# Kernel optimization log

Hardware: AMD Instinct MI355X
Metric: run time of the kernel (lower is better)

Reference implementation:

```python
import jax, jax.numpy as jnp
import numpy as np

N_NODES = 100000
N_EDGES = 1600000
IN_C = 64
HID = 64


def _glorot(key, shape):
    fan_in, fan_out = shape[1], shape[0]
    lim = (6.0 / (fan_in + fan_out)) ** 0.5
    return jax.random.uniform(key, shape, jnp.float32, -lim, lim)


def setup_inputs() -> dict:
    key = jax.random.key(0)
    ks = jax.random.split(key, 8)
    x = jax.random.normal(ks[0], (N_NODES, IN_C), jnp.float32)
    edge_index = jax.random.randint(ks[1], (2, N_EDGES), 0, N_NODES, jnp.int32)
    return {
        "x": x,
        "edge_index": edge_index,
        # conv1 (SAGEConv in->hid): lin_l (bias), lin_r (no bias)
        "W1l": _glorot(ks[2], (HID, IN_C)),
        "b1l": jnp.zeros((HID,), jnp.float32),
        "W1r": _glorot(ks[3], (HID, IN_C)),
        # conv2 (SAGEConv hid->hid)
        "W2l": _glorot(ks[4], (HID, HID)),
        "b2l": jnp.zeros((HID,), jnp.float32),
        "W2r": _glorot(ks[5], (HID, HID)),
        # edge scorer: Linear(2*hid, 1)
        "Wlin": _glorot(ks[6], (1, 2 * HID)),
        "blin": jnp.zeros((1,), jnp.float32),
    }


def _sage_conv(x, src, dst, Wl, bl, Wr, n_nodes):
    # mean aggregation of source features onto destination nodes
    agg = jax.ops.segment_sum(x[src], dst, num_segments=n_nodes)  # [N, F]
    cnt = jax.ops.segment_sum(jnp.ones((src.shape[0],), x.dtype), dst,
                              num_segments=n_nodes)  # [N]
    mean = agg / jnp.maximum(cnt, 1.0)[:, None]  # isolated nodes -> 0
    return mean @ Wl.T + bl + x @ Wr.T


def reference(x, edge_index, W1l, b1l, W1r, W2l, b2l, W2r, Wlin, blin):
    src, dst = edge_index[0], edge_index[1]
    n = x.shape[0]
    h = jax.nn.relu(_sage_conv(x, src, dst, W1l, b1l, W1r, n))
    h = jax.nn.relu(_sage_conv(h, src, dst, W2l, b2l, W2r, n))
    he = jnp.concatenate([h[src], h[dst]], axis=1)  # [E, 2*HID]
    return (he @ Wlin.T + blin).squeeze(-1)  # [E]
```

## Files before the change

kernel.cpp:

```cpp
#include <hip/hip_runtime.h>
#include <hip/hip_bf16.h>

#define N_NODES 100000
#define N_EDGES 1600000
#define NBUCK 196
#define BCAP 12288
#define CHUNK 4096
#define PART_BLOCKS 391
#define CONV_BLOCKS 6250
#define CAP32 32
#define QNODES 128
#define QCAP 3072
#define MSTRIDE 36


typedef __hip_bfloat16 bf16;
typedef short short8 __attribute__((ext_vector_type(8)));
typedef float f32x4 __attribute__((ext_vector_type(4)));
typedef unsigned int uint;

__device__ __forceinline__ short f2bs(float f) {
    bf16 h = __float2bfloat16(f);
    short s; __builtin_memcpy(&s, &h, 2); return s;
}
__device__ __forceinline__ float lo_bf(uint w) {
    uint v = w << 16; float f; __builtin_memcpy(&f, &v, 4); return f;
}
__device__ __forceinline__ float hi_bf(uint w) {
    uint v = w & 0xFFFF0000u; float f; __builtin_memcpy(&f, &v, 4); return f;
}
__device__ __forceinline__ uint pack2(float a, float b) {
    return (uint)(unsigned short)f2bs(a) | ((uint)(unsigned short)f2bs(b) << 16);
}
__device__ __forceinline__ short8 load8bf(const bf16* __restrict__ p, long idx) {
    return *(const short8*)((const short*)p + idx);
}

__global__ __launch_bounds__(256) void prep_kernel(
    const float* __restrict__ x, bf16* __restrict__ xb,
    const float* __restrict__ W1l, const float* __restrict__ W1r,
    const float* __restrict__ W2l, const float* __restrict__ W2r,
    bf16* __restrict__ wb,
    const int* __restrict__ src, const int* __restrict__ dst,
    int* __restrict__ gcur, int* __restrict__ pk)
{
    __shared__ int pl[256 * CAP32];
    __shared__ int cnt[256], gb[256];
    int t = threadIdx.x;

    if (blockIdx.x >= PART_BLOCKS) {
        int cb = blockIdx.x - PART_BLOCKS;
        int i = cb * 256 + t;
        float4 v = ((const float4*)x)[i];
        uint2 o;
        o.x = pack2(v.x, v.y);
        o.y = pack2(v.z, v.w);
        ((uint2*)xb)[i] = o;
        if (cb == 0) {
            for (int k = t; k < 16384; k += 256) {
                float vv;
                if (k < 4096)       vv = W1l[k];
                else if (k < 8192)  vv = W1r[k - 4096];
                else if (k < 12288) vv = W2l[k - 8192];
                else                vv = W2r[k - 12288];
                wb[k] = __float2bfloat16(vv);
            }
        }
        return;
    }

    cnt[t] = 0;
    __syncthreads();
    int e0 = blockIdx.x * CHUNK;
    for (int i = t; i < CHUNK; i += 256) {
        int e = e0 + i;
        if (e < N_EDGES) {
            int d = dst[e];
            int b = d >> 9;
            int payload = src[e] | ((d & 511) << 17);
            int p = atomicAdd(&cnt[b], 1);
            if (p < CAP32) {
                pl[b * CAP32 + p] = payload;
            } else {
                int g = atomicAdd(&gcur[b], 1);
                if (g < BCAP) pk[b * BCAP + g] = payload;
            }
        }
    }
    __syncthreads();
    {
        int c = cnt[t] < CAP32 ? cnt[t] : CAP32;
        gb[t] = c > 0 ? atomicAdd(&gcur[t], c) : 0;
        cnt[t] = c;
    }
    __syncthreads();
    for (int i = t; i < 256 * CAP32; i += 256) {
        int b = i >> 5;
        int pos = i & (CAP32 - 1);
        if (pos < cnt[b]) {
            int g = gb[b] + pos;
            if (g < BCAP) pk[b * BCAP + g] = pl[i];
        }
    }
}

__global__ __launch_bounds__(512) void csr_build(
    const int* __restrict__ gcur, const int* __restrict__ pk,
    int* __restrict__ csr, int2* __restrict__ node_range)
{
    __shared__ int deg[512], scn[512];
    __shared__ int cur[QNODES];
    __shared__ int csr_l[QCAP];
    int t = threadIdx.x;
    int b = blockIdx.x >> 2;
    int q = blockIdx.x & 3;
    int base = b * BCAP;
    int cnt = gcur[b];
    if (cnt > BCAP) cnt = BCAP;
    deg[t] = 0;
    __syncthreads();
    for (int i = t; i < cnt; i += 512)
        atomicAdd(&deg[pk[base + i] >> 17], 1);
    __syncthreads();
    if (t < 64) {
        int e[8], inc[8], s = 0;
#pragma unroll
        for (int k = 0; k < 8; k++) { e[k] = deg[t * 8 + k]; s += e[k]; inc[k] = s; }
        int run = s;
#pragma unroll
        for (int off = 1; off < 64; off <<= 1) {
            int u = __shfl_up(run, off);
            if (t >= off) run += u;
        }
        int excl = run - s;
#pragma unroll
        for (int k = 0; k < 8; k++) scn[t * 8 + k] = excl + inc[k];
    }
    __syncthreads();
    int hs = q * QNODES;
    int hend = hs + QNODES;
    int hs_excl = scn[hs] - deg[hs];
    int he_excl = (hend < 512) ? (scn[hend] - deg[hend]) : cnt;
    int qcnt = he_excl - hs_excl;
    int excl = scn[t] - deg[t];
    if (t >= hs && t < hend) {
        cur[t - hs] = excl - hs_excl;
        int n = (b << 9) + t;
        if (n < N_NODES) node_range[n] = make_int2(base + excl, base + excl + deg[t]);
    }
    __syncthreads();
    for (int i = t; i < cnt; i += 512) {
        int v = pk[base + i];
        int ld = v >> 17;
        if (ld >= hs && ld < hend) {
            int p = atomicAdd(&cur[ld - hs], 1);
            if (p < QCAP) csr_l[p] = v & 0x1FFFF;
        }
    }
    __syncthreads();
    for (int i = t; i < qcnt && i < QCAP; i += 512)
        csr[base + hs_excl + i] = csr_l[i];
}


__device__ __forceinline__ void gather_mean_lds(
    const bf16* __restrict__ feat, const int2* __restrict__ node_range,
    const int* __restrict__ csr, int nb0, uint* __restrict__ mean_l)
{
    int wave = threadIdx.x >> 6, lane = threadIdx.x & 63;
    int g = lane >> 3, ci = lane & 7;
    int nl = wave * 8 + g;
    int n = nb0 + nl;
    int2 rg = (n < N_NODES) ? node_range[n] : make_int2(0, 0);
    int beg = rg.x, end = rg.y;
    const uint* fw = (const uint*)feat;
    float a0 = 0.f, a1 = 0.f, a2 = 0.f, a3 = 0.f;
    float a4 = 0.f, a5 = 0.f, a6 = 0.f, a7 = 0.f;
    int i = beg;
    for (; i + 7 < end; i += 8) {
        int s0 = csr[i],     s1 = csr[i + 1], s2 = csr[i + 2], s3 = csr[i + 3];
        int s4 = csr[i + 4], s5 = csr[i + 5], s6 = csr[i + 6], s7 = csr[i + 7];
        uint4 w0 = *(const uint4*)(fw + (long)s0 * 32 + ci * 4);
        uint4 w1 = *(const uint4*)(fw + (long)s1 * 32 + ci * 4);
        uint4 w2 = *(const uint4*)(fw + (long)s2 * 32 + ci * 4);
        uint4 w3 = *(const uint4*)(fw + (long)s3 * 32 + ci * 4);
        uint4 w4 = *(const uint4*)(fw + (long)s4 * 32 + ci * 4);
        uint4 w5 = *(const uint4*)(fw + (long)s5 * 32 + ci * 4);
        uint4 w6 = *(const uint4*)(fw + (long)s6 * 32 + ci * 4);
        uint4 w7 = *(const uint4*)(fw + (long)s7 * 32 + ci * 4);
        a0 += lo_bf(w0.x) + lo_bf(w1.x) + lo_bf(w2.x) + lo_bf(w3.x)
            + lo_bf(w4.x) + lo_bf(w5.x) + lo_bf(w6.x) + lo_bf(w7.x);
        a1 += hi_bf(w0.x) + hi_bf(w1.x) + hi_bf(w2.x) + hi_bf(w3.x)
            + hi_bf(w4.x) + hi_bf(w5.x) + hi_bf(w6.x) + hi_bf(w7.x);
        a2 += lo_bf(w0.y) + lo_bf(w1.y) + lo_bf(w2.y) + lo_bf(w3.y)
            + lo_bf(w4.y) + lo_bf(w5.y) + lo_bf(w6.y) + lo_bf(w7.y);
        a3 += hi_bf(w0.y) + hi_bf(w1.y) + hi_bf(w2.y) + hi_bf(w3.y)
            + hi_bf(w4.y) + hi_bf(w5.y) + hi_bf(w6.y) + hi_bf(w7.y);
        a4 += lo_bf(w0.z) + lo_bf(w1.z) + lo_bf(w2.z) + lo_bf(w3.z)
            + lo_bf(w4.z) + lo_bf(w5.z) + lo_bf(w6.z) + lo_bf(w7.z);
        a5 += hi_bf(w0.z) + hi_bf(w1.z) + hi_bf(w2.z) + hi_bf(w3.z)
            + hi_bf(w4.z) + hi_bf(w5.z) + hi_bf(w6.z) + hi_bf(w7.z);
        a6 += lo_bf(w0.w) + lo_bf(w1.w) + lo_bf(w2.w) + lo_bf(w3.w)
            + lo_bf(w4.w) + lo_bf(w5.w) + lo_bf(w6.w) + lo_bf(w7.w);
        a7 += hi_bf(w0.w) + hi_bf(w1.w) + hi_bf(w2.w) + hi_bf(w3.w)
            + hi_bf(w4.w) + hi_bf(w5.w) + hi_bf(w6.w) + hi_bf(w7.w);
    }
    for (; i + 1 < end; i += 2) {
        int s0 = csr[i], s1 = csr[i + 1];
        uint4 w0 = *(const uint4*)(fw + (long)s0 * 32 + ci * 4);
        uint4 w1 = *(const uint4*)(fw + (long)s1 * 32 + ci * 4);
        a0 += lo_bf(w0.x) + lo_bf(w1.x); a1 += hi_bf(w0.x) + hi_bf(w1.x);
        a2 += lo_bf(w0.y) + lo_bf(w1.y); a3 += hi_bf(w0.y) + hi_bf(w1.y);
        a4 += lo_bf(w0.z) + lo_bf(w1.z); a5 += hi_bf(w0.z) + hi_bf(w1.z);
        a6 += lo_bf(w0.w) + lo_bf(w1.w); a7 += hi_bf(w0.w) + hi_bf(w1.w);
    }
    if (i < end) {
        int s = csr[i];
        uint4 w = *(const uint4*)(fw + (long)s * 32 + ci * 4);
        a0 += lo_bf(w.x); a1 += hi_bf(w.x);
        a2 += lo_bf(w.y); a3 += hi_bf(w.y);
        a4 += lo_bf(w.z); a5 += hi_bf(w.z);
        a6 += lo_bf(w.w); a7 += hi_bf(w.w);
    }
    int d = end - beg;
    float inv = d > 0 ? 1.0f / (float)d : 0.0f;
    uint4 qv;
    qv.x = pack2(a0 * inv, a1 * inv);
    qv.y = pack2(a2 * inv, a3 * inv);
    qv.z = pack2(a4 * inv, a5 * inv);
    qv.w = pack2(a6 * inv, a7 * inv);
    *(uint4*)(mean_l + nl * MSTRIDE + ci * 4) = qv;
}

__device__ __forceinline__ short8 load_bfrag(
    const bf16* __restrict__ wlb, int f, int c, int quad)
{
    if (c < 2) return load8bf(wlb, (long)f * 64 + c * 32 + quad * 8);
    return load8bf(wlb, 4096 + (long)f * 64 + (c - 2) * 32 + quad * 8);
}

__global__ __launch_bounds__(512) void layer1_fused(
    const bf16* __restrict__ xb, const int2* __restrict__ nrng,
    const int* __restrict__ csr, const bf16* __restrict__ wlb,
    const float* __restrict__ bl, bf16* __restrict__ h_out)
{
    __shared__ uint mean_l[64 * MSTRIDE];
    int nb0 = blockIdx.x * 64;
    gather_mean_lds(xb, nrng, csr, nb0, mean_l);
    __syncthreads();
    int tid = threadIdx.x;
    int wave = tid >> 6, lane = tid & 63;
    if (wave >= 4) return;
    int quad = lane >> 4, n16 = lane & 15;
    int nb = nb0 + wave * 16;
    int ln = wave * 16 + n16;

    int node_a = nb + n16;
    int na = node_a < N_NODES ? node_a : N_NODES - 1;
    short8 a[4];
#pragma unroll
    for (int c = 0; c < 2; c++)
        a[c] = *(const short8*)(mean_l + ln * MSTRIDE + c * 16 + quad * 4);
#pragma unroll
    for (int c = 0; c < 2; c++)
        a[2 + c] = load8bf(xb, (long)na * 64 + c * 32 + quad * 8);

#pragma unroll
    for (int t = 0; t < 4; t++) {
        int f = 16 * t + n16;
        f32x4 acc = {0.f, 0.f, 0.f, 0.f};
#pragma unroll
        for (int c = 0; c < 4; c++) {
            short8 b = load_bfrag(wlb, f, c, quad);
            acc = __builtin_amdgcn_mfma_f32_16x16x32_bf16(a[c], b, acc, 0, 0, 0);
        }
        float bias = bl[f];
#pragma unroll
        for (int r = 0; r < 4; r++) {
            int node = nb + quad * 4 + r;
            if (node < N_NODES)
                h_out[(long)node * 64 + f] = __float2bfloat16(fmaxf(acc[r] + bias, 0.0f));
        }
    }
}

__global__ __launch_bounds__(512) void layer2_fused(
    const bf16* __restrict__ h1, const int2* __restrict__ nrng,
    const int* __restrict__ csr, const bf16* __restrict__ wlb,
    const float* __restrict__ bl, const float* __restrict__ Wlin,
    float* __restrict__ s_src, float* __restrict__ s_dst)
{
    __shared__ uint mean_l[64 * MSTRIDE];
    int nb0 = blockIdx.x * 64;
    gather_mean_lds(h1, nrng, csr, nb0, mean_l);
    __syncthreads();
    int tid = threadIdx.x;
    int wave = tid >> 6, lane = tid & 63;
    if (wave >= 4) return;
    int quad = lane >> 4, n16 = lane & 15;
    int nb = nb0 + wave * 16;
    int ln = wave * 16 + n16;

    int node_a = nb + n16;
    int na = node_a < N_NODES ? node_a : N_NODES - 1;
    short8 a[4];
#pragma unroll
    for (int c = 0; c < 2; c++)
        a[c] = *(const short8*)(mean_l + ln * MSTRIDE + c * 16 + quad * 4);
#pragma unroll
    for (int c = 0; c < 2; c++)
        a[2 + c] = load8bf(h1, (long)na * 64 + c * 32 + quad * 8);

    float sa[4] = {0.f, 0.f, 0.f, 0.f};
    float sb[4] = {0.f, 0.f, 0.f, 0.f};
#pragma unroll
    for (int t = 0; t < 4; t++) {
        int f = 16 * t + n16;
        f32x4 acc = {0.f, 0.f, 0.f, 0.f};
#pragma unroll
        for (int c = 0; c < 4; c++) {
            short8 b = load_bfrag(wlb, f, c, quad);
            acc = __builtin_amdgcn_mfma_f32_16x16x32_bf16(a[c], b, acc, 0, 0, 0);
        }
        float bias = bl[f];
        float wa = Wlin[f];
        float wb = Wlin[64 + f];
#pragma unroll
        for (int r = 0; r < 4; r++) {
            float h = fmaxf(acc[r] + bias, 0.0f);
            sa[r] += h * wa;
            sb[r] += h * wb;
        }
    }
#pragma unroll
    for (int m = 1; m < 16; m <<= 1) {
#pragma unroll
        for (int r = 0; r < 4; r++) {
            sa[r] += __shfl_xor(sa[r], m);
            sb[r] += __shfl_xor(sb[r], m);
        }
    }
    if (n16 == 0) {
#pragma unroll
        for (int r = 0; r < 4; r++) {
            int node = nb + quad * 4 + r;
            if (node < N_NODES) { s_src[node] = sa[r]; s_dst[node] = sb[r]; }
        }
    }
}

__global__ __launch_bounds__(256) void edge_out_kernel(
    const int* __restrict__ src, const int* __restrict__ dst,
    const float* __restrict__ s_src, const float* __restrict__ s_dst,
    const float* __restrict__ blin, float* __restrict__ out)
{
    int i = blockIdx.x * 256 + threadIdx.x;
    if (i >= N_EDGES / 4) return;
    int4 s4 = ((const int4*)src)[i];
    int4 d4 = ((const int4*)dst)[i];
    float b = blin[0];
    float4 o;
    o.x = s_src[s4.x] + s_dst[d4.x] + b;
    o.y = s_src[s4.y] + s_dst[d4.y] + b;
    o.z = s_src[s4.z] + s_dst[d4.z] + b;
    o.w = s_src[s4.w] + s_dst[d4.w] + b;
    ((float4*)out)[i] = o;
}

extern "C" void kernel_launch(void* const* d_in, const int* in_sizes, int n_in,
                              void* d_out, int out_size, void* d_ws, size_t ws_size,
                              hipStream_t stream) {
    const float* x    = (const float*)d_in[0];
    const int*   ei   = (const int*)d_in[1];
    const float* W1l  = (const float*)d_in[2];
    const float* b1l  = (const float*)d_in[3];
    const float* W1r  = (const float*)d_in[4];
    const float* W2l  = (const float*)d_in[5];
    const float* b2l  = (const float*)d_in[6];
    const float* W2r  = (const float*)d_in[7];
    const float* Wlin = (const float*)d_in[8];
    const float* blin = (const float*)d_in[9];
    float* out = (float*)d_out;

    const int* src = ei;
    const int* dst = ei + N_EDGES;

    char* w = (char*)d_ws;
    bf16*  xb    = (bf16*)w;  w += (size_t)N_NODES * 64 * 2;
    bf16*  h1    = (bf16*)w;  w += (size_t)N_NODES * 64 * 2;
    float* ssrc  = (float*)w; w += (size_t)N_NODES * 4;
    float* sdst  = (float*)w; w += (size_t)N_NODES * 4;
    int2*  nrng  = (int2*)w;  w += (size_t)N_NODES * 8;
    int*   gcur  = (int*)w;   w += 256 * 4;
    bf16*  wb    = (bf16*)w;  w += 16384 * 2;
    int*   pk    = (int*)w;   w += (size_t)NBUCK * BCAP * 4;
    int*   csr   = (int*)w;   w += (size_t)NBUCK * BCAP * 4;

    const int prep_blocks  = PART_BLOCKS + CONV_BLOCKS;
    const int csr_blocks   = NBUCK * 4;
    const int fused_blocks = (N_NODES + 63) / 64;
    const int eo_blocks    = (N_EDGES / 4 + 255) / 256;

    (void)hipMemsetAsync(gcur, 0, 256 * 4, stream);
    prep_kernel<<<prep_blocks, 256, 0, stream>>>(
        x, xb, W1l, W1r, W2l, W2r, wb, src, dst, gcur, pk);
    csr_build<<<csr_blocks, 512, 0, stream>>>(gcur, pk, csr, nrng);

    layer1_fused<<<fused_blocks, 512, 0, stream>>>(xb, nrng, csr, wb, b1l, h1);
    layer2_fused<<<fused_blocks, 512, 0, stream>>>(h1, nrng, csr, wb + 8192, b2l, Wlin, ssrc, sdst);

    edge_out_kernel<<<eo_blocks, 256, 0, stream>>>(src, dst, ssrc, sdst, blin, out);
}
```

Baseline: 235.0 us.

## Fuse CSR build into layer kernels via per-block LDS adjacency lists

Removes the separate csr_build kernel and the global CSR/node_range arrays. Each layer kernel now scans its bucket's packed edges from pk and builds per-node neighbor lists in shared memory (capped at 96 per node) before gathering features. This saves one launch and the global CSR write and read, but each layer block rescans the whole bucket (8x redundant scans per bucket, twice across both layers), uses more LDS per block, and silently truncates nodes with more than 96 in-edges.

```diff
diff --git a/kernel.cpp b/kernel.cpp
--- a/kernel.cpp
+++ b/kernel.cpp
@@ -9,8 +9,7 @@
 #define PART_BLOCKS 391
 #define CONV_BLOCKS 6250
 #define CAP32 32
-#define QNODES 128
-#define QCAP 3072
+#define LCAP 96
 #define MSTRIDE 36
 
 
@@ -104,82 +103,41 @@
     }
 }
 
-__global__ __launch_bounds__(512) void csr_build(
-    const int* __restrict__ gcur, const int* __restrict__ pk,
-    int* __restrict__ csr, int2* __restrict__ node_range)
-{
-    __shared__ int deg[512], scn[512];
-    __shared__ int cur[QNODES];
-    __shared__ int csr_l[QCAP];
+
+__device__ __forceinline__ void build_and_gather(
+    const bf16* __restrict__ feat, const int* __restrict__ gcur,
+    const int* __restrict__ pk, int b, int hs,
+    int* __restrict__ lists_l, int* __restrict__ cnt_l, uint* __restrict__ mean_l)
+{
     int t = threadIdx.x;
-    int b = blockIdx.x >> 2;
-    int q = blockIdx.x & 3;
+    if (t < 64) cnt_l[t] = 0;
+    __syncthreads();
     int base = b * BCAP;
     int cnt = gcur[b];
     if (cnt > BCAP) cnt = BCAP;
-    deg[t] = 0;
-    __syncthreads();
-    for (int i = t; i < cnt; i += 512)
-        atomicAdd(&deg[pk[base + i] >> 17], 1);
-    __syncthreads();
-    if (t < 64) {
-        int e[8], inc[8], s = 0;
-#pragma unroll
-        for (int k = 0; k < 8; k++) { e[k] = deg[t * 8 + k]; s += e[k]; inc[k] = s; }
-        int run = s;
-#pragma unroll
-        for (int off = 1; off < 64; off <<= 1) {
-            int u = __shfl_up(run, off);
-            if (t >= off) run += u;
-        }
-        int excl = run - s;
-#pragma unroll
-        for (int k = 0; k < 8; k++) scn[t * 8 + k] = excl + inc[k];
-    }
-    __syncthreads();
-    int hs = q * QNODES;
-    int hend = hs + QNODES;
-    int hs_excl = scn[hs] - deg[hs];
-    int he_excl = (hend < 512) ? (scn[hend] - deg[hend]) : cnt;
-    int qcnt = he_excl - hs_excl;
-    int excl = scn[t] - deg[t];
-    if (t >= hs && t < hend) {
-        cur[t - hs] = excl - hs_excl;
-        int n = (b << 9) + t;
-        if (n < N_NODES) node_range[n] = make_int2(base + excl, base + excl + deg[t]);
-    }
-    __syncthreads();
     for (int i = t; i < cnt; i += 512) {
         int v = pk[base + i];
-        int ld = v >> 17;
-        if (ld >= hs && ld < hend) {
-            int p = atomicAdd(&cur[ld - hs], 1);
-            if (p < QCAP) csr_l[p] = v & 0x1FFFF;
-        }
-    }
-    __syncthreads();
-    for (int i = t; i < qcnt && i < QCAP; i += 512)
-        csr[base + hs_excl + i] = csr_l[i];
-}
-
-
-__device__ __forceinline__ void gather_mean_lds(
-    const bf16* __restrict__ feat, const int2* __restrict__ node_range,
-    const int* __restrict__ csr, int nb0, uint* __restrict__ mean_l)
-{
-    int wave = threadIdx.x >> 6, lane = threadIdx.x & 63;
+        int ld = (v >> 17) - hs;
+        if ((unsigned)ld < 64u) {
+            int p = atomicAdd(&cnt_l[ld], 1);
+            if (p < LCAP) lists_l[ld * LCAP + p] = v & 0x1FFFF;
+        }
+    }
+    __syncthreads();
+
+    int wave = t >> 6, lane = t & 63;
     int g = lane >> 3, ci = lane & 7;
     int nl = wave * 8 + g;
-    int n = nb0 + nl;
-    int2 rg = (n < N_NODES) ? node_range[n] : make_int2(0, 0);
-    int beg = rg.x, end = rg.y;
+    int deg = cnt_l[nl];
+    if (deg > LCAP) deg = LCAP;
+    const int* lst = lists_l + nl * LCAP;
     const uint* fw = (const uint*)feat;
     float a0 = 0.f, a1 = 0.f, a2 = 0.f, a3 = 0.f;
     float a4 = 0.f, a5 = 0.f, a6 = 0.f, a7 = 0.f;
-    int i = beg;
-    for (; i + 7 < end; i += 8) {
-        int s0 = csr[i],     s1 = csr[i + 1], s2 = csr[i + 2], s3 = csr[i + 3];
-        int s4 = csr[i + 4], s5 = csr[i + 5], s6 = csr[i + 6], s7 = csr[i + 7];
+    int i = 0;
+    for (; i + 7 < deg; i += 8) {
+        int s0 = lst[i],     s1 = lst[i + 1], s2 = lst[i + 2], s3 = lst[i + 3];
+        int s4 = lst[i + 4], s5 = lst[i + 5], s6 = lst[i + 6], s7 = lst[i + 7];
         uint4 w0 = *(const uint4*)(fw + (long)s0 * 32 + ci * 4);
         uint4 w1 = *(const uint4*)(fw + (long)s1 * 32 + ci * 4);
         uint4 w2 = *(const uint4*)(fw + (long)s2 * 32 + ci * 4);
@@ -205,8 +163,8 @@
         a7 += hi_bf(w0.w) + hi_bf(w1.w) + hi_bf(w2.w) + hi_bf(w3.w)
             + hi_bf(w4.w) + hi_bf(w5.w) + hi_bf(w6.w) + hi_bf(w7.w);
     }
-    for (; i + 1 < end; i += 2) {
-        int s0 = csr[i], s1 = csr[i + 1];
+    for (; i + 1 < deg; i += 2) {
+        int s0 = lst[i], s1 = lst[i + 1];
         uint4 w0 = *(const uint4*)(fw + (long)s0 * 32 + ci * 4);
         uint4 w1 = *(const uint4*)(fw + (long)s1 * 32 + ci * 4);
         a0 += lo_bf(w0.x) + lo_bf(w1.x); a1 += hi_bf(w0.x) + hi_bf(w1.x);
@@ -214,16 +172,15 @@
         a4 += lo_bf(w0.z) + lo_bf(w1.z); a5 += hi_bf(w0.z) + hi_bf(w1.z);
         a6 += lo_bf(w0.w) + lo_bf(w1.w); a7 += hi_bf(w0.w) + hi_bf(w1.w);
     }
-    if (i < end) {
-        int s = csr[i];
+    if (i < deg) {
+        int s = lst[i];
         uint4 w = *(const uint4*)(fw + (long)s * 32 + ci * 4);
         a0 += lo_bf(w.x); a1 += hi_bf(w.x);
         a2 += lo_bf(w.y); a3 += hi_bf(w.y);
         a4 += lo_bf(w.z); a5 += hi_bf(w.z);
         a6 += lo_bf(w.w); a7 += hi_bf(w.w);
     }
-    int d = end - beg;
-    float inv = d > 0 ? 1.0f / (float)d : 0.0f;
+    float inv = deg > 0 ? 1.0f / (float)deg : 0.0f;
     uint4 qv;
     qv.x = pack2(a0 * inv, a1 * inv);
     qv.y = pack2(a2 * inv, a3 * inv);
@@ -240,13 +197,17 @@
 }
 
 __global__ __launch_bounds__(512) void layer1_fused(
-    const bf16* __restrict__ xb, const int2* __restrict__ nrng,
-    const int* __restrict__ csr, const bf16* __restrict__ wlb,
+    const bf16* __restrict__ xb, const int* __restrict__ gcur,
+    const int* __restrict__ pk, const bf16* __restrict__ wlb,
     const float* __restrict__ bl, bf16* __restrict__ h_out)
 {
+    __shared__ int lists_l[64 * LCAP];
+    __shared__ int cnt_l[64];
     __shared__ uint mean_l[64 * MSTRIDE];
-    int nb0 = blockIdx.x * 64;
-    gather_mean_lds(xb, nrng, csr, nb0, mean_l);
+    int b = blockIdx.x >> 3;
+    int hs = (blockIdx.x & 7) * 64;
+    int nb0 = (b << 9) + hs;
+    build_and_gather(xb, gcur, pk, b, hs, lists_l, cnt_l, mean_l);
     __syncthreads();
     int tid = threadIdx.x;
     int wave = tid >> 6, lane = tid & 63;
@@ -271,8 +232,8 @@
         f32x4 acc = {0.f, 0.f, 0.f, 0.f};
 #pragma unroll
         for (int c = 0; c < 4; c++) {
-            short8 b = load_bfrag(wlb, f, c, quad);
-            acc = __builtin_amdgcn_mfma_f32_16x16x32_bf16(a[c], b, acc, 0, 0, 0);
+            short8 bfr = load_bfrag(wlb, f, c, quad);
+            acc = __builtin_amdgcn_mfma_f32_16x16x32_bf16(a[c], bfr, acc, 0, 0, 0);
         }
         float bias = bl[f];
 #pragma unroll
@@ -285,14 +246,18 @@
 }
 
 __global__ __launch_bounds__(512) void layer2_fused(
-    const bf16* __restrict__ h1, const int2* __restrict__ nrng,
-    const int* __restrict__ csr, const bf16* __restrict__ wlb,
+    const bf16* __restrict__ h1, const int* __restrict__ gcur,
+    const int* __restrict__ pk, const bf16* __restrict__ wlb,
     const float* __restrict__ bl, const float* __restrict__ Wlin,
     float* __restrict__ s_src, float* __restrict__ s_dst)
 {
+    __shared__ int lists_l[64 * LCAP];
+    __shared__ int cnt_l[64];
     __shared__ uint mean_l[64 * MSTRIDE];
-    int nb0 = blockIdx.x * 64;
-    gather_mean_lds(h1, nrng, csr, nb0, mean_l);
+    int b = blockIdx.x >> 3;
+    int hs = (blockIdx.x & 7) * 64;
+    int nb0 = (b << 9) + hs;
+    build_and_gather(h1, gcur, pk, b, hs, lists_l, cnt_l, mean_l);
     __syncthreads();
     int tid = threadIdx.x;
     int wave = tid >> 6, lane = tid & 63;
@@ -319,8 +284,8 @@
         f32x4 acc = {0.f, 0.f, 0.f, 0.f};
 #pragma unroll
         for (int c = 0; c < 4; c++) {
-            short8 b = load_bfrag(wlb, f, c, quad);
-            acc = __builtin_amdgcn_mfma_f32_16x16x32_bf16(a[c], b, acc, 0, 0, 0);
+            short8 bfr = load_bfrag(wlb, f, c, quad);
+            acc = __builtin_amdgcn_mfma_f32_16x16x32_bf16(a[c], bfr, acc, 0, 0, 0);
         }
         float bias = bl[f];
         float wa = Wlin[f];
@@ -390,24 +355,20 @@
     bf16*  h1    = (bf16*)w;  w += (size_t)N_NODES * 64 * 2;
     float* ssrc  = (float*)w; w += (size_t)N_NODES * 4;
     float* sdst  = (float*)w; w += (size_t)N_NODES * 4;
-    int2*  nrng  = (int2*)w;  w += (size_t)N_NODES * 8;
     int*   gcur  = (int*)w;   w += 256 * 4;
     bf16*  wb    = (bf16*)w;  w += 16384 * 2;
     int*   pk    = (int*)w;   w += (size_t)NBUCK * BCAP * 4;
-    int*   csr   = (int*)w;   w += (size_t)NBUCK * BCAP * 4;
 
     const int prep_blocks  = PART_BLOCKS + CONV_BLOCKS;
-    const int csr_blocks   = NBUCK * 4;
-    const int fused_blocks = (N_NODES + 63) / 64;
+    const int fused_blocks = NBUCK * 8;
     const int eo_blocks    = (N_EDGES / 4 + 255) / 256;
 
     (void)hipMemsetAsync(gcur, 0, 256 * 4, stream);
     prep_kernel<<<prep_blocks, 256, 0, stream>>>(
         x, xb, W1l, W1r, W2l, W2r, wb, src, dst, gcur, pk);
-    csr_build<<<csr_blocks, 512, 0, stream>>>(gcur, pk, csr, nrng);
-
-    layer1_fused<<<fused_blocks, 512, 0, stream>>>(xb, nrng, csr, wb, b1l, h1);
-    layer2_fused<<<fused_blocks, 512, 0, stream>>>(h1, nrng, csr, wb + 8192, b2l, Wlin, ssrc, sdst);
+
+    layer1_fused<<<fused_blocks, 512, 0, stream>>>(xb, gcur, pk, wb, b1l, h1);
+    layer2_fused<<<fused_blocks, 512, 0, stream>>>(h1, gcur, pk, wb + 8192, b2l, Wlin, ssrc, sdst);
 
     edge_out_kernel<<<eo_blocks, 256, 0, stream>>>(src, dst, ssrc, sdst, blin, out);
 }
```

Result: slower. 254.3 us (+8.2%).

## Fuse all stages into one cooperative persistent kernel with grid syncs

Applied to the files above, without the earlier changes.

Replaces the memset and five separate kernel launches with a single cooperative kernel on 512 blocks. The kernel runs partitioning, CSR build, both SAGE layers and the edge scoring as grid-stride phases separated by grid.sync(), with the old launch sequence kept as a fallback if the cooperative launch fails. The aim is to remove launch gaps and per-kernel tail effects. In exchange every phase is capped at 512 blocks of 512 threads, which may lower parallelism and latency hiding in the gather-heavy layers, and each grid-wide barrier adds its own cost.

```diff
diff --git a/kernel.cpp b/kernel.cpp
--- a/kernel.cpp
+++ b/kernel.cpp
@@ -1,5 +1,8 @@
 #include <hip/hip_runtime.h>
 #include <hip/hip_bf16.h>
+#include <hip/hip_cooperative_groups.h>
+
+namespace cg = cooperative_groups;
 
 #define N_NODES 100000
 #define N_EDGES 1600000
@@ -8,10 +11,13 @@
 #define CHUNK 4096
 #define PART_BLOCKS 391
 #define CONV_BLOCKS 6250
+#define XGROUPS 1600000
 #define CAP32 32
 #define QNODES 128
 #define QCAP 3072
 #define MSTRIDE 36
+#define GRID_BLOCKS 512
+#define NWIN 1563
 
 
 typedef __hip_bfloat16 bf16;
@@ -35,133 +41,6 @@
 __device__ __forceinline__ short8 load8bf(const bf16* __restrict__ p, long idx) {
     return *(const short8*)((const short*)p + idx);
 }
-
-__global__ __launch_bounds__(256) void prep_kernel(
-    const float* __restrict__ x, bf16* __restrict__ xb,
-    const float* __restrict__ W1l, const float* __restrict__ W1r,
-    const float* __restrict__ W2l, const float* __restrict__ W2r,
-    bf16* __restrict__ wb,
-    const int* __restrict__ src, const int* __restrict__ dst,
-    int* __restrict__ gcur, int* __restrict__ pk)
-{
-    __shared__ int pl[256 * CAP32];
-    __shared__ int cnt[256], gb[256];
-    int t = threadIdx.x;
-
-    if (blockIdx.x >= PART_BLOCKS) {
-        int cb = blockIdx.x - PART_BLOCKS;
-        int i = cb * 256 + t;
-        float4 v = ((const float4*)x)[i];
-        uint2 o;
-        o.x = pack2(v.x, v.y);
-        o.y = pack2(v.z, v.w);
-        ((uint2*)xb)[i] = o;
-        if (cb == 0) {
-            for (int k = t; k < 16384; k += 256) {
-                float vv;
-                if (k < 4096)       vv = W1l[k];
-                else if (k < 8192)  vv = W1r[k - 4096];
-                else if (k < 12288) vv = W2l[k - 8192];
-                else                vv = W2r[k - 12288];
-                wb[k] = __float2bfloat16(vv);
-            }
-        }
-        return;
-    }
-
-    cnt[t] = 0;
-    __syncthreads();
-    int e0 = blockIdx.x * CHUNK;
-    for (int i = t; i < CHUNK; i += 256) {
-        int e = e0 + i;
-        if (e < N_EDGES) {
-            int d = dst[e];
-            int b = d >> 9;
-            int payload = src[e] | ((d & 511) << 17);
-            int p = atomicAdd(&cnt[b], 1);
-            if (p < CAP32) {
-                pl[b * CAP32 + p] = payload;
-            } else {
-                int g = atomicAdd(&gcur[b], 1);
-                if (g < BCAP) pk[b * BCAP + g] = payload;
-            }
-        }
-    }
-    __syncthreads();
-    {
-        int c = cnt[t] < CAP32 ? cnt[t] : CAP32;
-        gb[t] = c > 0 ? atomicAdd(&gcur[t], c) : 0;
-        cnt[t] = c;
-    }
-    __syncthreads();
-    for (int i = t; i < 256 * CAP32; i += 256) {
-        int b = i >> 5;
-        int pos = i & (CAP32 - 1);
-        if (pos < cnt[b]) {
-            int g = gb[b] + pos;
-            if (g < BCAP) pk[b * BCAP + g] = pl[i];
-        }
-    }
-}
-
-__global__ __launch_bounds__(512) void csr_build(
-    const int* __restrict__ gcur, const int* __restrict__ pk,
-    int* __restrict__ csr, int2* __restrict__ node_range)
-{
-    __shared__ int deg[512], scn[512];
-    __shared__ int cur[QNODES];
-    __shared__ int csr_l[QCAP];
-    int t = threadIdx.x;
-    int b = blockIdx.x >> 2;
-    int q = blockIdx.x & 3;
-    int base = b * BCAP;
-    int cnt = gcur[b];
-    if (cnt > BCAP) cnt = BCAP;
-    deg[t] = 0;
-    __syncthreads();
-    for (int i = t; i < cnt; i += 512)
-        atomicAdd(&deg[pk[base + i] >> 17], 1);
-    __syncthreads();
-    if (t < 64) {
-        int e[8], inc[8], s = 0;
-#pragma unroll
-        for (int k = 0; k < 8; k++) { e[k] = deg[t * 8 + k]; s += e[k]; inc[k] = s; }
-        int run = s;
-#pragma unroll
-        for (int off = 1; off < 64; off <<= 1) {
-            int u = __shfl_up(run, off);
-            if (t >= off) run += u;
-        }
-        int excl = run - s;
-#pragma unroll
-        for (int k = 0; k < 8; k++) scn[t * 8 + k] = excl + inc[k];
-    }
-    __syncthreads();
-    int hs = q * QNODES;
-    int hend = hs + QNODES;
-    int hs_excl = scn[hs] - deg[hs];
-    int he_excl = (hend < 512) ? (scn[hend] - deg[hend]) : cnt;
-    int qcnt = he_excl - hs_excl;
-    int excl = scn[t] - deg[t];
-    if (t >= hs && t < hend) {
-        cur[t - hs] = excl - hs_excl;
-        int n = (b << 9) + t;
-        if (n < N_NODES) node_range[n] = make_int2(base + excl, base + excl + deg[t]);
-    }
-    __syncthreads();
-    for (int i = t; i < cnt; i += 512) {
-        int v = pk[base + i];
-        int ld = v >> 17;
-        if (ld >= hs && ld < hend) {
-            int p = atomicAdd(&cur[ld - hs], 1);
-            if (p < QCAP) csr_l[p] = v & 0x1FFFF;
-        }
-    }
-    __syncthreads();
-    for (int i = t; i < qcnt && i < QCAP; i += 512)
-        csr[base + hs_excl + i] = csr_l[i];
-}
-
 
 __device__ __forceinline__ void gather_mean_lds(
     const bf16* __restrict__ feat, const int2* __restrict__ node_range,
@@ -239,6 +118,385 @@
     return load8bf(wlb, 4096 + (long)f * 64 + (c - 2) * 32 + quad * 8);
 }
 
+__global__ __launch_bounds__(512, 4) void mega_kernel(
+    const float* __restrict__ x, const int* __restrict__ ei,
+    const float* __restrict__ W1l, const float* __restrict__ b1l,
+    const float* __restrict__ W1r, const float* __restrict__ W2l,
+    const float* __restrict__ b2l, const float* __restrict__ W2r,
+    const float* __restrict__ Wlin, const float* __restrict__ blin,
+    float* __restrict__ out,
+    bf16* __restrict__ xb, bf16* __restrict__ h1,
+    float* __restrict__ ssrc, float* __restrict__ sdst,
+    int2* __restrict__ nrng, int* __restrict__ gcur,
+    bf16* __restrict__ wb, int* __restrict__ pk, int* __restrict__ csr)
+{
+    cg::grid_group grid = cg::this_grid();
+    __shared__ int smem[8704];
+    const int* src = ei;
+    const int* dst = ei + N_EDGES;
+    int t = threadIdx.x;
+    int bid = blockIdx.x;
+
+    if (bid == 0 && t < 256) gcur[t] = 0;
+    grid.sync();
+
+    {
+        for (int i = bid * 512 + t; i < XGROUPS; i += GRID_BLOCKS * 512) {
+            float4 v = ((const float4*)x)[i];
+            uint2 o;
+            o.x = pack2(v.x, v.y);
+            o.y = pack2(v.z, v.w);
+            ((uint2*)xb)[i] = o;
+        }
+        if (bid == GRID_BLOCKS - 1) {
+            for (int k = t; k < 16384; k += 512) {
+                float vv;
+                if (k < 4096)       vv = W1l[k];
+                else if (k < 8192)  vv = W1r[k - 4096];
+                else if (k < 12288) vv = W2l[k - 8192];
+                else                vv = W2r[k - 12288];
+                wb[k] = __float2bfloat16(vv);
+            }
+        }
+        if (bid < PART_BLOCKS) {
+            int* pl  = smem;
+            int* cnt = smem + 8192;
+            int* gb  = smem + 8448;
+            if (t < 256) cnt[t] = 0;
+            __syncthreads();
+            int e0 = bid * CHUNK;
+            for (int i = t; i < CHUNK; i += 512) {
+                int e = e0 + i;
+                if (e < N_EDGES) {
+                    int d = dst[e];
+                    int b = d >> 9;
+                    int payload = src[e] | ((d & 511) << 17);
+                    int p = atomicAdd(&cnt[b], 1);
+                    if (p < CAP32) {
+                        pl[b * CAP32 + p] = payload;
+                    } else {
+                        int g = atomicAdd(&gcur[b], 1);
+                        if (g < BCAP) pk[b * BCAP + g] = payload;
+                    }
+                }
+            }
+            __syncthreads();
+            if (t < 256) {
+                int c = cnt[t] < CAP32 ? cnt[t] : CAP32;
+                gb[t] = c > 0 ? atomicAdd(&gcur[t], c) : 0;
+                cnt[t] = c;
+            }
+            __syncthreads();
+            for (int i = t; i < 256 * CAP32; i += 512) {
+                int b = i >> 5;
+                int pos = i & (CAP32 - 1);
+                if (pos < cnt[b]) {
+                    int g = gb[b] + pos;
+                    if (g < BCAP) pk[b * BCAP + g] = pl[i];
+                }
+            }
+        }
+    }
+    grid.sync();
+
+    for (int qb = bid; qb < NBUCK * 4; qb += GRID_BLOCKS) {
+        int* deg   = smem;
+        int* scn   = smem + 512;
+        int* cur   = smem + 1024;
+        int* csr_l = smem + 1152;
+        int b = qb >> 2;
+        int q = qb & 3;
+        int base = b * BCAP;
+        int cnt = gcur[b];
+        if (cnt > BCAP) cnt = BCAP;
+        deg[t] = 0;
+        __syncthreads();
+        for (int i = t; i < cnt; i += 512)
+            atomicAdd(&deg[pk[base + i] >> 17], 1);
+        __syncthreads();
+        if (t < 64) {
+            int e[8], inc[8], s = 0;
+#pragma unroll
+            for (int k = 0; k < 8; k++) { e[k] = deg[t * 8 + k]; s += e[k]; inc[k] = s; }
+            int run = s;
+#pragma unroll
+            for (int off = 1; off < 64; off <<= 1) {
+                int u = __shfl_up(run, off);
+                if (t >= off) run += u;
+            }
+            int excl = run - s;
+#pragma unroll
+            for (int k = 0; k < 8; k++) scn[t * 8 + k] = excl + inc[k];
+        }
+        __syncthreads();
+        int hs = q * QNODES;
+        int hend = hs + QNODES;
+        int hs_excl = scn[hs] - deg[hs];
+        int he_excl = (hend < 512) ? (scn[hend] - deg[hend]) : cnt;
+        int qcnt = he_excl - hs_excl;
+        int excl = scn[t] - deg[t];
+        if (t >= hs && t < hend) {
+            cur[t - hs] = excl - hs_excl;
+            int n = (b << 9) + t;
+            if (n < N_NODES) nrng[n] = make_int2(base + excl, base + excl + deg[t]);
+        }
+        __syncthreads();
+        for (int i = t; i < cnt; i += 512) {
+            int v = pk[base + i];
+            int ld = v >> 17;
+            if (ld >= hs && ld < hend) {
+                int p = atomicAdd(&cur[ld - hs], 1);
+                if (p < QCAP) csr_l[p] = v & 0x1FFFF;
+            }
+        }
+        __syncthreads();
+        for (int i = t; i < qcnt && i < QCAP; i += 512)
+            csr[base + hs_excl + i] = csr_l[i];
+        __syncthreads();
+    }
+    grid.sync();
+
+    for (int w = bid; w < NWIN; w += GRID_BLOCKS) {
+        uint* mean_l = (uint*)smem;
+        int nb0 = w * 64;
+        gather_mean_lds(xb, nrng, csr, nb0, mean_l);
+        __syncthreads();
+        int wave = t >> 6, lane = t & 63;
+        if (wave < 4) {
+            int quad = lane >> 4, n16 = lane & 15;
+            int nb = nb0 + wave * 16;
+            int ln = wave * 16 + n16;
+            int node_a = nb + n16;
+            int na = node_a < N_NODES ? node_a : N_NODES - 1;
+            short8 a[4];
+#pragma unroll
+            for (int c = 0; c < 2; c++)
+                a[c] = *(const short8*)(mean_l + ln * MSTRIDE + c * 16 + quad * 4);
+#pragma unroll
+            for (int c = 0; c < 2; c++)
+                a[2 + c] = load8bf(xb, (long)na * 64 + c * 32 + quad * 8);
+#pragma unroll
+            for (int tt = 0; tt < 4; tt++) {
+                int f = 16 * tt + n16;
+                f32x4 acc = {0.f, 0.f, 0.f, 0.f};
+#pragma unroll
+                for (int c = 0; c < 4; c++) {
+                    short8 bfr = load_bfrag(wb, f, c, quad);
+                    acc = __builtin_amdgcn_mfma_f32_16x16x32_bf16(a[c], bfr, acc, 0, 0, 0);
+                }
+                float bias = b1l[f];
+#pragma unroll
+                for (int r = 0; r < 4; r++) {
+                    int node = nb + quad * 4 + r;
+                    if (node < N_NODES)
+                        h1[(long)node * 64 + f] = __float2bfloat16(fmaxf(acc[r] + bias, 0.0f));
+                }
+            }
+        }
+        __syncthreads();
+    }
+    grid.sync();
+
+    for (int w = bid; w < NWIN; w += GRID_BLOCKS) {
+        uint* mean_l = (uint*)smem;
+        int nb0 = w * 64;
+        gather_mean_lds(h1, nrng, csr, nb0, mean_l);
+        __syncthreads();
+        int wave = t >> 6, lane = t & 63;
+        if (wave < 4) {
+            int quad = lane >> 4, n16 = lane & 15;
+            int nb = nb0 + wave * 16;
+            int ln = wave * 16 + n16;
+            int node_a = nb + n16;
+            int na = node_a < N_NODES ? node_a : N_NODES - 1;
+            short8 a[4];
+#pragma unroll
+            for (int c = 0; c < 2; c++)
+                a[c] = *(const short8*)(mean_l + ln * MSTRIDE + c * 16 + quad * 4);
+#pragma unroll
+            for (int c = 0; c < 2; c++)
+                a[2 + c] = load8bf(h1, (long)na * 64 + c * 32 + quad * 8);
+            float sa[4] = {0.f, 0.f, 0.f, 0.f};
+            float sb[4] = {0.f, 0.f, 0.f, 0.f};
+            const bf16* wlb = wb + 8192;
+#pragma unroll
+            for (int tt = 0; tt < 4; tt++) {
+                int f = 16 * tt + n16;
+                f32x4 acc = {0.f, 0.f, 0.f, 0.f};
+#pragma unroll
+                for (int c = 0; c < 4; c++) {
+                    short8 bfr = load_bfrag(wlb, f, c, quad);
+                    acc = __builtin_amdgcn_mfma_f32_16x16x32_bf16(a[c], bfr, acc, 0, 0, 0);
+                }
+                float bias = b2l[f];
+                float wa = Wlin[f];
+                float wbv = Wlin[64 + f];
+#pragma unroll
+                for (int r = 0; r < 4; r++) {
+                    float h = fmaxf(acc[r] + bias, 0.0f);
+                    sa[r] += h * wa;
+                    sb[r] += h * wbv;
+                }
+            }
+#pragma unroll
+            for (int m = 1; m < 16; m <<= 1) {
+#pragma unroll
+                for (int r = 0; r < 4; r++) {
+                    sa[r] += __shfl_xor(sa[r], m);
+                    sb[r] += __shfl_xor(sb[r], m);
+                }
+            }
+            if (n16 == 0) {
+#pragma unroll
+                for (int r = 0; r < 4; r++) {
+                    int node = nb + quad * 4 + r;
+                    if (node < N_NODES) { ssrc[node] = sa[r]; sdst[node] = sb[r]; }
+                }
+            }
+        }
+        __syncthreads();
+    }
+    grid.sync();
+
+    for (int i = bid * 512 + t; i < N_EDGES / 4; i += GRID_BLOCKS * 512) {
+        int4 s4 = ((const int4*)src)[i];
+        int4 d4 = ((const int4*)dst)[i];
+        float b = blin[0];
+        float4 o;
+        o.x = ssrc[s4.x] + sdst[d4.x] + b;
+        o.y = ssrc[s4.y] + sdst[d4.y] + b;
+        o.z = ssrc[s4.z] + sdst[d4.z] + b;
+        o.w = ssrc[s4.w] + sdst[d4.w] + b;
+        ((float4*)out)[i] = o;
+    }
+}
+
+__global__ __launch_bounds__(256) void prep_kernel(
+    const float* __restrict__ x, bf16* __restrict__ xb,
+    const float* __restrict__ W1l, const float* __restrict__ W1r,
+    const float* __restrict__ W2l, const float* __restrict__ W2r,
+    bf16* __restrict__ wb,
+    const int* __restrict__ src, const int* __restrict__ dst,
+    int* __restrict__ gcur, int* __restrict__ pk)
+{
+    __shared__ int pl[256 * CAP32];
+    __shared__ int cnt[256], gb[256];
+    int t = threadIdx.x;
+
+    if (blockIdx.x >= PART_BLOCKS) {
+        int cb = blockIdx.x - PART_BLOCKS;
+        int i = cb * 256 + t;
+        float4 v = ((const float4*)x)[i];
+        uint2 o;
+        o.x = pack2(v.x, v.y);
+        o.y = pack2(v.z, v.w);
+        ((uint2*)xb)[i] = o;
+        if (cb == 0) {
+            for (int k = t; k < 16384; k += 256) {
+                float vv;
+                if (k < 4096)       vv = W1l[k];
+                else if (k < 8192)  vv = W1r[k - 4096];
+                else if (k < 12288) vv = W2l[k - 8192];
+                else                vv = W2r[k - 12288];
+                wb[k] = __float2bfloat16(vv);
+            }
+        }
+        return;
+    }
+
+    cnt[t] = 0;
+    __syncthreads();
+    int e0 = blockIdx.x * CHUNK;
+    for (int i = t; i < CHUNK; i += 256) {
+        int e = e0 + i;
+        if (e < N_EDGES) {
+            int d = dst[e];
+            int b = d >> 9;
+            int payload = src[e] | ((d & 511) << 17);
+            int p = atomicAdd(&cnt[b], 1);
+            if (p < CAP32) {
+                pl[b * CAP32 + p] = payload;
+            } else {
+                int g = atomicAdd(&gcur[b], 1);
+                if (g < BCAP) pk[b * BCAP + g] = payload;
+            }
+        }
+    }
+    __syncthreads();
+    {
+        int c = cnt[t] < CAP32 ? cnt[t] : CAP32;
+        gb[t] = c > 0 ? atomicAdd(&gcur[t], c) : 0;
+        cnt[t] = c;
+    }
+    __syncthreads();
+    for (int i = t; i < 256 * CAP32; i += 256) {
+        int b = i >> 5;
+        int pos = i & (CAP32 - 1);
+        if (pos < cnt[b]) {
+            int g = gb[b] + pos;
+            if (g < BCAP) pk[b * BCAP + g] = pl[i];
+        }
+    }
+}
+
+__global__ __launch_bounds__(512) void csr_build(
+    const int* __restrict__ gcur, const int* __restrict__ pk,
+    int* __restrict__ csr, int2* __restrict__ node_range)
+{
+    __shared__ int deg[512], scn[512];
+    __shared__ int cur[QNODES];
+    __shared__ int csr_l[QCAP];
+    int t = threadIdx.x;
+    int b = blockIdx.x >> 2;
+    int q = blockIdx.x & 3;
+    int base = b * BCAP;
+    int cnt = gcur[b];
+    if (cnt > BCAP) cnt = BCAP;
+    deg[t] = 0;
+    __syncthreads();
+    for (int i = t; i < cnt; i += 512)
+        atomicAdd(&deg[pk[base + i] >> 17], 1);
+    __syncthreads();
+    if (t < 64) {
+        int e[8], inc[8], s = 0;
+#pragma unroll
+        for (int k = 0; k < 8; k++) { e[k] = deg[t * 8 + k]; s += e[k]; inc[k] = s; }
+        int run = s;
+#pragma unroll
+        for (int off = 1; off < 64; off <<= 1) {
+            int u = __shfl_up(run, off);
+            if (t >= off) run += u;
+        }
+        int excl = run - s;
+#pragma unroll
+        for (int k = 0; k < 8; k++) scn[t * 8 + k] = excl + inc[k];
+    }
+    __syncthreads();
+    int hs = q * QNODES;
+    int hend = hs + QNODES;
+    int hs_excl = scn[hs] - deg[hs];
+    int he_excl = (hend < 512) ? (scn[hend] - deg[hend]) : cnt;
+    int qcnt = he_excl - hs_excl;
+    int excl = scn[t] - deg[t];
+    if (t >= hs && t < hend) {
+        cur[t - hs] = excl - hs_excl;
+        int n = (b << 9) + t;
+        if (n < N_NODES) node_range[n] = make_int2(base + excl, base + excl + deg[t]);
+    }
+    __syncthreads();
+    for (int i = t; i < cnt; i += 512) {
+        int v = pk[base + i];
+        int ld = v >> 17;
+        if (ld >= hs && ld < hend) {
+            int p = atomicAdd(&cur[ld - hs], 1);
+            if (p < QCAP) csr_l[p] = v & 0x1FFFF;
+        }
+    }
+    __syncthreads();
+    for (int i = t; i < qcnt && i < QCAP; i += 512)
+        csr[base + hs_excl + i] = csr_l[i];
+}
+
 __global__ __launch_bounds__(512) void layer1_fused(
     const bf16* __restrict__ xb, const int2* __restrict__ nrng,
     const int* __restrict__ csr, const bf16* __restrict__ wlb,
@@ -271,8 +529,8 @@
         f32x4 acc = {0.f, 0.f, 0.f, 0.f};
 #pragma unroll
         for (int c = 0; c < 4; c++) {
-            short8 b = load_bfrag(wlb, f, c, quad);
-            acc = __builtin_amdgcn_mfma_f32_16x16x32_bf16(a[c], b, acc, 0, 0, 0);
+            short8 bfr = load_bfrag(wlb, f, c, quad);
+            acc = __builtin_amdgcn_mfma_f32_16x16x32_bf16(a[c], bfr, acc, 0, 0, 0);
         }
         float bias = bl[f];
 #pragma unroll
@@ -319,8 +577,8 @@
         f32x4 acc = {0.f, 0.f, 0.f, 0.f};
 #pragma unroll
         for (int c = 0; c < 4; c++) {
-            short8 b = load_bfrag(wlb, f, c, quad);
-            acc = __builtin_amdgcn_mfma_f32_16x16x32_bf16(a[c], b, acc, 0, 0, 0);
+            short8 bfr = load_bfrag(wlb, f, c, quad);
+            acc = __builtin_amdgcn_mfma_f32_16x16x32_bf16(a[c], bfr, acc, 0, 0, 0);
         }
         float bias = bl[f];
         float wa = Wlin[f];
@@ -396,18 +654,26 @@
     int*   pk    = (int*)w;   w += (size_t)NBUCK * BCAP * 4;
     int*   csr   = (int*)w;   w += (size_t)NBUCK * BCAP * 4;
 
-    const int prep_blocks  = PART_BLOCKS + CONV_BLOCKS;
-    const int csr_blocks   = NBUCK * 4;
-    const int fused_blocks = (N_NODES + 63) / 64;
-    const int eo_blocks    = (N_EDGES / 4 + 255) / 256;
-
-    (void)hipMemsetAsync(gcur, 0, 256 * 4, stream);
-    prep_kernel<<<prep_blocks, 256, 0, stream>>>(
-        x, xb, W1l, W1r, W2l, W2r, wb, src, dst, gcur, pk);
-    csr_build<<<csr_blocks, 512, 0, stream>>>(gcur, pk, csr, nrng);
-
-    layer1_fused<<<fused_blocks, 512, 0, stream>>>(xb, nrng, csr, wb, b1l, h1);
-    layer2_fused<<<fused_blocks, 512, 0, stream>>>(h1, nrng, csr, wb + 8192, b2l, Wlin, ssrc, sdst);
-
-    edge_out_kernel<<<eo_blocks, 256, 0, stream>>>(src, dst, ssrc, sdst, blin, out);
-}
+    void* args[] = {
+        (void*)&x, (void*)&ei, (void*)&W1l, (void*)&b1l, (void*)&W1r,
+        (void*)&W2l, (void*)&b2l, (void*)&W2r, (void*)&Wlin, (void*)&blin,
+        (void*)&out, (void*)&xb, (void*)&h1, (void*)&ssrc, (void*)&sdst,
+        (void*)&nrng, (void*)&gcur, (void*)&wb, (void*)&pk, (void*)&csr
+    };
+    hipError_t err = hipLaunchCooperativeKernel((const void*)mega_kernel,
+                                                dim3(GRID_BLOCKS), dim3(512),
+                                                args, 0, stream);
+    if (err != hipSuccess) {
+        const int prep_blocks  = PART_BLOCKS + CONV_BLOCKS;
+        const int csr_blocks   = NBUCK * 4;
+        const int fused_blocks = (N_NODES + 63) / 64;
+        const int eo_blocks    = (N_EDGES / 4 + 255) / 256;
+        (void)hipMemsetAsync(gcur, 0, 256 * 4, stream);
+        prep_kernel<<<prep_blocks, 256, 0, stream>>>(
+            x, xb, W1l, W1r, W2l, W2r, wb, src, dst, gcur, pk);
+        csr_build<<<csr_blocks, 512, 0, stream>>>(gcur, pk, csr, nrng);
+        layer1_fused<<<fused_blocks, 512, 0, stream>>>(xb, nrng, csr, wb, b1l, h1);
+        layer2_fused<<<fused_blocks, 512, 0, stream>>>(h1, nrng, csr, wb + 8192, b2l, Wlin, ssrc, sdst);
+        edge_out_kernel<<<eo_blocks, 256, 0, stream>>>(src, dst, ssrc, sdst, blin, out);
+    }
+}
```

Result: slower. 518.4 us (+120.5%).
